# Kernel optimization log

Hardware: AMD Instinct MI355X
Metric: run time of the kernel (lower is better)

Reference implementation:

```python
import jax, jax.numpy as jnp
import numpy as np

K = 9  # kernel_size (knn neighbors, loop=True -> self included)

def setup_inputs() -> dict:
    key = jax.random.key(0)
    k1, k2, k3 = jax.random.split(key, 3)
    B, C, H, W = 8, 64, 32, 32
    OUT = 64
    x = jax.random.normal(k1, (B, C, H, W), dtype=jnp.float32)
    # SAGEConv params: lin_l (neighbor aggregate, with bias), lin_r (root, no bias)
    s = 1.0 / np.sqrt(C)
    W_l = jax.random.uniform(k2, (OUT, C), minval=-s, maxval=s, dtype=jnp.float32)
    b_l = jnp.zeros((OUT,), dtype=jnp.float32)
    W_r = jax.random.uniform(k3, (OUT, C), minval=-s, maxval=s, dtype=jnp.float32)
    return {"x": x, "W_l": W_l, "b_l": b_l, "W_r": W_r}

def _knn_mean(x_f, batches):
    # squared-euclidean pairwise distances [N, N], masked across batches
    sq = jnp.sum(x_f * x_f, axis=-1)
    dist = sq[:, None] + sq[None, :] - 2.0 * (x_f @ x_f.T)
    cross = batches[:, None] != batches[None, :]
    dist = jnp.where(cross, jnp.inf, dist)
    neg, idx = jax.lax.top_k(-dist, K)          # k nearest (self included, dist 0)
    valid = (neg != -jnp.inf).astype(x_f.dtype)  # handle degenerate last-batch node
    nbr = x_f[idx] * valid[..., None]            # [N, K, C]
    return nbr.sum(axis=1) / valid.sum(axis=1, keepdims=True)

def reference(x, W_l, b_l, W_r):
    B, C, H, Wd = x.shape
    N = B * H * Wd
    x_f = x.transpose(0, 2, 3, 1).reshape(N, C)  # flat_nodes: [B*H*W, C]
    # torch.linspace(0, B, steps=N).to(int64): truncation of i*B/(N-1)
    batches = jnp.linspace(0.0, float(B), N).astype(jnp.int32)
    mean_nbr = _knn_mean(x_f, batches)
    # SAGEConv: lin_l(mean_j x_j) + lin_r(x_i)
    return mean_nbr @ W_l.T + b_l + x_f @ W_r.T
```

## Files before the change

kernel.cpp:

```cpp
#include <hip/hip_runtime.h>
#include <cstdint>
#include <cstddef>


#define CBUF_HW (64 * 1028)
#define CBUF_BYTES (CBUF_HW * 2)

__device__ __forceinline__ unsigned mono32(float d) {
  unsigned u = __float_as_uint(d);
  return (u & 0x80000000u) ? ~u : (u | 0x80000000u);
}

__device__ __forceinline__ unsigned bmin32(unsigned v) {
#pragma unroll
  for (int off = 32; off; off >>= 1) {
    unsigned o = (unsigned)__shfl_xor((int)v, off, 64);
    v = (o < v) ? o : v;
  }
  return v;
}

__device__ __forceinline__ float rdlane(float v, int src) {
  return __int_as_float(__builtin_amdgcn_readlane(__float_as_int(v), src));
}

__device__ __forceinline__ unsigned short bf16rn(float v) {
  unsigned bits = __float_as_uint(v);
  return (unsigned short)((bits + 0x7FFFu + ((bits >> 16) & 1u)) >> 16);
}

extern "C" __global__ __launch_bounds__(256, 1)
void k_fused(const float* __restrict__ x,
             const float* __restrict__ Wl,
             const float* __restrict__ bl,
             const float* __restrict__ Wr,
             float* __restrict__ out) {
  extern __shared__ unsigned short cbuf[];
  int t = threadIdx.x;
  int lane = t & 63;
  int w = t >> 6;
  int n0 = (int)blockIdx.x << 5;
  int s = (n0 >= 7168) ? 7168 : (n0 & ~1023);
  int b = s >> 10;
  const float* xb = x + ((size_t)b << 16);

  float rowf[8];
#pragma unroll
  for (int r = 0; r < 8; ++r) {
    int n = n0 + (w << 3) + r;
    rowf[r] = xb[(lane << 10) + (n & 1023)];
  }

  float acc[8][16];
#pragma unroll
  for (int r = 0; r < 8; ++r)
#pragma unroll
    for (int q = 0; q < 16; ++q) acc[r][q] = 0.f;
  float sqc[16];
#pragma unroll
  for (int q = 0; q < 16; ++q) sqc[q] = 0.f;

  float4 cnd[2][4];
#pragma unroll
  for (int e = 0; e < 4; ++e)
    cnd[0][e] = *(const float4*)&xb[(lane << 2) + (e << 8)];

#pragma unroll 1
  for (int ch2 = 0; ch2 < 32; ++ch2) {
#pragma unroll
    for (int h = 0; h < 2; ++h) {
      int ch = (ch2 << 1) + h;
      int cur = ch & 1;
      if ((ch & 7) == 0) __syncthreads();
      int chn = (ch < 63) ? ch + 1 : 63;
#pragma unroll
      for (int e = 0; e < 4; ++e)
        cnd[cur ^ 1][e] = *(const float4*)&xb[(chn << 10) + (lane << 2) + (e << 8)];
      if ((ch >> 4) == w) {
#pragma unroll
        for (int e = 0; e < 4; ++e) {
          ushort4 pk;
          pk.x = bf16rn(cnd[cur][e].x);
          pk.y = bf16rn(cnd[cur][e].y);
          pk.z = bf16rn(cnd[cur][e].z);
          pk.w = bf16rn(cnd[cur][e].w);
          *(ushort4*)&cbuf[ch * 1028 + (lane << 2) + (e << 8)] = pk;
        }
      }
      float rv[8];
#pragma unroll
      for (int r = 0; r < 8; ++r) rv[r] = rdlane(rowf[r], ch);
#pragma unroll
      for (int e = 0; e < 4; ++e) {
        float cv[4] = {cnd[cur][e].x, cnd[cur][e].y, cnd[cur][e].z, cnd[cur][e].w};
#pragma unroll
        for (int j = 0; j < 4; ++j) {
          int q = (e << 2) + j;
          sqc[q] = fmaf(cv[j], cv[j], sqc[q]);
#pragma unroll
          for (int r = 0; r < 8; ++r)
            acc[r][q] = fmaf(rv[r], cv[j], acc[r][q]);
        }
      }
    }
  }
  __syncthreads();

  float ms[8];
#pragma unroll
  for (int r = 0; r < 8; ++r) {
    int n = n0 + (w << 3) + r;
    if (n == 8191) { ms[r] = rowf[r]; continue; }
    int lr = n - s;
    int lslot = (((lr >> 8) << 2) | (lr & 3));
    int llane = (lr >> 2) & 63;
    float sel = sqc[0];
#pragma unroll
    for (int q = 1; q < 16; ++q) sel = (q == lslot) ? sqc[q] : sel;
    float sqr = __shfl(sel, llane, 64);

    bool mrow = (s == 7168);
    unsigned d[16];
#pragma unroll
    for (int q = 0; q < 16; ++q)
      d[q] = mono32((sqr + sqc[q]) - 2.f * acc[r][q]);
    if (mrow && lane == 63) d[15] = 0xFFFFFFFFu;

    unsigned m1d = d[0], m2d = d[1];
    int m1s = 0, m2s = 1;
    if (m2d < m1d) { unsigned td = m1d; m1d = m2d; m2d = td; m1s = 1; m2s = 0; }
#pragma unroll
    for (int q = 2; q < 16; ++q) {
      unsigned dq = d[q];
      bool lt1 = dq < m1d, lt2 = dq < m2d;
      m2d = lt1 ? m1d : (lt2 ? dq : m2d);
      m2s = lt1 ? m1s : (lt2 ? q : m2s);
      m1d = lt1 ? dq : m1d;
      m1s = lt1 ? q : m1s;
    }
    unsigned lmd = m1d;
    int lms = m1s;
    unsigned rmask = 0;
    bool stale = false;
    float msum = 0.f;
#pragma unroll 1
    for (int kk = 0; kk < 9; ++kk) {
      unsigned g = bmin32(lmd);
      bool eq = (lmd == g);
      unsigned long long mask = __ballot(eq);
      unsigned cc = ((unsigned)lane << 2) | ((unsigned)(lms >> 2) << 8) | (unsigned)(lms & 3);
      unsigned wc;
      if (__popcll(mask) == 1) {
        wc = (unsigned)__shfl((int)cc, (int)(__ffsll((long long)mask) - 1), 64);
      } else {
        unsigned tc = eq ? cc : 0xFFFFFFFFu;
        wc = bmin32(tc);
      }
      msum += __uint_as_float((unsigned)cbuf[lane * 1028 + (int)wc] << 16);
      if (eq && cc == wc) {
        rmask |= 1u << lms;
        if (!stale) { lmd = m2d; lms = m2s; stale = true; }
        else {
          unsigned bd = 0xFFFFFFFFu; int bs = 0;
#pragma unroll
          for (int q = 0; q < 16; ++q) {
            bool alive = ((rmask >> q) & 1u) == 0u;
            bool take = alive && (d[q] < bd);
            bd = take ? d[q] : bd;
            bs = take ? q : bs;
          }
          lmd = bd; lms = bs;
        }
      }
    }
    ms[r] = msum / 9.0f;
  }

  float4 wl4[16], wr4[16];
#pragma unroll
  for (int k = 0; k < 16; ++k) {
    wl4[k] = *(const float4*)&Wl[(lane << 6) + (k << 2)];
    wr4[k] = *(const float4*)&Wr[(lane << 6) + (k << 2)];
  }
  float bias = bl[lane];
#pragma unroll 1
  for (int r = 0; r < 8; ++r) {
    int n = n0 + (w << 3) + r;
    float accL = 0.f, accR = 0.f;
#pragma unroll
    for (int c = 0; c < 64; ++c) {
      float mc = rdlane(ms[r], c);
      float xc = rdlane(rowf[r], c);
      const float* wlp = (const float*)&wl4[c >> 2];
      const float* wrp = (const float*)&wr4[c >> 2];
      accL = fmaf(mc, wlp[c & 3], accL);
      accR = fmaf(xc, wrp[c & 3], accR);
    }
    out[((size_t)n << 6) + lane] = accL + accR + bias;
  }
}

extern "C" void kernel_launch(void* const* d_in, const int* in_sizes, int n_in,
                              void* d_out, int out_size, void* d_ws, size_t ws_size,
                              hipStream_t stream) {
  const float* x  = (const float*)d_in[0];
  const float* Wl = (const float*)d_in[1];
  const float* bl = (const float*)d_in[2];
  const float* Wr = (const float*)d_in[3];
  float* out = (float*)d_out;

  hipFuncSetAttribute((const void*)k_fused,
                      hipFuncAttributeMaxDynamicSharedMemorySize, CBUF_BYTES);
  k_fused<<<256, 256, CBUF_BYTES, stream>>>(x, Wl, bl, Wr, out);
}
```

Baseline: 118.6 us.

## Interleave top-k selection across eight rows and prefetch two channels per step

The top-9 selection loop now processes all eight rows of a warp together, interleaving their butterfly shuffle reductions so the independent shuffle chains can overlap instead of running serially per row. The tie-break path always uses a second min-reduction rather than branching on ballot popcount. The candidate prefetch is restructured to load two channels per outer iteration, and the periodic __syncthreads inside the distance loop is removed. This raises register pressure (8x16 distance array kept live), and dropping the barriers relies on only the final sync before the LDS reads.

```diff
diff --git a/kernel.cpp b/kernel.cpp
--- a/kernel.cpp
+++ b/kernel.cpp
@@ -3,21 +3,12 @@
 #include <cstddef>
 
 
-#define CBUF_HW (64 * 1028)
-#define CBUF_BYTES (CBUF_HW * 2)
+#define CBUF_STRIDE 1028
+#define CBUF_BYTES (64 * CBUF_STRIDE * 2)
 
 __device__ __forceinline__ unsigned mono32(float d) {
   unsigned u = __float_as_uint(d);
   return (u & 0x80000000u) ? ~u : (u | 0x80000000u);
-}
-
-__device__ __forceinline__ unsigned bmin32(unsigned v) {
-#pragma unroll
-  for (int off = 32; off; off >>= 1) {
-    unsigned o = (unsigned)__shfl_xor((int)v, off, 64);
-    v = (o < v) ? o : v;
-  }
-  return v;
 }
 
 __device__ __forceinline__ float rdlane(float v, int src) {
@@ -41,8 +32,7 @@
   int w = t >> 6;
   int n0 = (int)blockIdx.x << 5;
   int s = (n0 >= 7168) ? 7168 : (n0 & ~1023);
-  int b = s >> 10;
-  const float* xb = x + ((size_t)b << 16);
+  const float* xb = x + ((size_t)(s >> 10) << 16);
 
   float rowf[8];
 #pragma unroll
@@ -60,31 +50,37 @@
 #pragma unroll
   for (int q = 0; q < 16; ++q) sqc[q] = 0.f;
 
-  float4 cnd[2][4];
-#pragma unroll
-  for (int e = 0; e < 4; ++e)
-    cnd[0][e] = *(const float4*)&xb[(lane << 2) + (e << 8)];
+  float4 pb[2][2][4];
+#pragma unroll
+  for (int h = 0; h < 2; ++h)
+#pragma unroll
+    for (int e = 0; e < 4; ++e)
+      pb[0][h][e] = *(const float4*)&xb[(h << 10) + (lane << 2) + (e << 8)];
 
 #pragma unroll 1
   for (int ch2 = 0; ch2 < 32; ++ch2) {
+    int cur = ch2 & 1;
+    if (ch2 < 31) {
+      int chn = (ch2 << 1) + 2;
+#pragma unroll
+      for (int h = 0; h < 2; ++h)
+#pragma unroll
+        for (int e = 0; e < 4; ++e)
+          pb[cur ^ 1][h][e] =
+              *(const float4*)&xb[((chn + h) << 10) + (lane << 2) + (e << 8)];
+    }
 #pragma unroll
     for (int h = 0; h < 2; ++h) {
       int ch = (ch2 << 1) + h;
-      int cur = ch & 1;
-      if ((ch & 7) == 0) __syncthreads();
-      int chn = (ch < 63) ? ch + 1 : 63;
-#pragma unroll
-      for (int e = 0; e < 4; ++e)
-        cnd[cur ^ 1][e] = *(const float4*)&xb[(chn << 10) + (lane << 2) + (e << 8)];
       if ((ch >> 4) == w) {
 #pragma unroll
         for (int e = 0; e < 4; ++e) {
           ushort4 pk;
-          pk.x = bf16rn(cnd[cur][e].x);
-          pk.y = bf16rn(cnd[cur][e].y);
-          pk.z = bf16rn(cnd[cur][e].z);
-          pk.w = bf16rn(cnd[cur][e].w);
-          *(ushort4*)&cbuf[ch * 1028 + (lane << 2) + (e << 8)] = pk;
+          pk.x = bf16rn(pb[cur][h][e].x);
+          pk.y = bf16rn(pb[cur][h][e].y);
+          pk.z = bf16rn(pb[cur][h][e].z);
+          pk.w = bf16rn(pb[cur][h][e].w);
+          *(ushort4*)&cbuf[ch * CBUF_STRIDE + (lane << 2) + (e << 8)] = pk;
         }
       }
       float rv[8];
@@ -92,7 +88,7 @@
       for (int r = 0; r < 8; ++r) rv[r] = rdlane(rowf[r], ch);
 #pragma unroll
       for (int e = 0; e < 4; ++e) {
-        float cv[4] = {cnd[cur][e].x, cnd[cur][e].y, cnd[cur][e].z, cnd[cur][e].w};
+        float cv[4] = {pb[cur][h][e].x, pb[cur][h][e].y, pb[cur][h][e].z, pb[cur][h][e].w};
 #pragma unroll
         for (int j = 0; j < 4; ++j) {
           int q = (e << 2) + j;
@@ -106,74 +102,116 @@
   }
   __syncthreads();
 
-  float ms[8];
-#pragma unroll
-  for (int r = 0; r < 8; ++r) {
-    int n = n0 + (w << 3) + r;
-    if (n == 8191) { ms[r] = rowf[r]; continue; }
-    int lr = n - s;
-    int lslot = (((lr >> 8) << 2) | (lr & 3));
+  float sqr[8];
+#pragma unroll
+  for (int r = 0; r < 8; ++r) {
+    int lr = (n0 + (w << 3) + r) - s;
+    int lslot = ((lr >> 8) << 2) | (lr & 3);
     int llane = (lr >> 2) & 63;
     float sel = sqc[0];
 #pragma unroll
     for (int q = 1; q < 16; ++q) sel = (q == lslot) ? sqc[q] : sel;
-    float sqr = __shfl(sel, llane, 64);
-
-    bool mrow = (s == 7168);
-    unsigned d[16];
+    sqr[r] = __shfl(sel, llane, 64);
+  }
+
+  bool mrow = (s == 7168);
+  unsigned du[8][16];
+#pragma unroll
+  for (int r = 0; r < 8; ++r)
 #pragma unroll
     for (int q = 0; q < 16; ++q)
-      d[q] = mono32((sqr + sqc[q]) - 2.f * acc[r][q]);
-    if (mrow && lane == 63) d[15] = 0xFFFFFFFFu;
-
-    unsigned m1d = d[0], m2d = d[1];
-    int m1s = 0, m2s = 1;
-    if (m2d < m1d) { unsigned td = m1d; m1d = m2d; m2d = td; m1s = 1; m2s = 0; }
+      du[r][q] = mono32((sqr[r] + sqc[q]) - 2.f * acc[r][q]);
+  if (mrow && lane == 63)
+#pragma unroll
+    for (int r = 0; r < 8; ++r) du[r][15] = 0xFFFFFFFFu;
+
+  unsigned m1d[8], m2d[8];
+  int m1s[8], m2s[8];
+#pragma unroll
+  for (int r = 0; r < 8; ++r) {
+    unsigned a = du[r][0], b = du[r][1];
+    if (b < a) { m1d[r] = b; m2d[r] = a; m1s[r] = 1; m2s[r] = 0; }
+    else       { m1d[r] = a; m2d[r] = b; m1s[r] = 0; m2s[r] = 1; }
 #pragma unroll
     for (int q = 2; q < 16; ++q) {
-      unsigned dq = d[q];
-      bool lt1 = dq < m1d, lt2 = dq < m2d;
-      m2d = lt1 ? m1d : (lt2 ? dq : m2d);
-      m2s = lt1 ? m1s : (lt2 ? q : m2s);
-      m1d = lt1 ? dq : m1d;
-      m1s = lt1 ? q : m1s;
-    }
-    unsigned lmd = m1d;
-    int lms = m1s;
-    unsigned rmask = 0;
-    bool stale = false;
-    float msum = 0.f;
+      unsigned dq = du[r][q];
+      bool lt1 = dq < m1d[r], lt2 = dq < m2d[r];
+      m2d[r] = lt1 ? m1d[r] : (lt2 ? dq : m2d[r]);
+      m2s[r] = lt1 ? m1s[r] : (lt2 ? q : m2s[r]);
+      m1d[r] = lt1 ? dq : m1d[r];
+      m1s[r] = lt1 ? q : m1s[r];
+    }
+  }
+
+  unsigned lmd[8], rmask[8];
+  int lms[8];
+  unsigned staleM = 0;
+  float msum[8];
+#pragma unroll
+  for (int r = 0; r < 8; ++r) {
+    lmd[r] = m1d[r]; lms[r] = m1s[r]; rmask[r] = 0u; msum[r] = 0.f;
+  }
+
 #pragma unroll 1
-    for (int kk = 0; kk < 9; ++kk) {
-      unsigned g = bmin32(lmd);
-      bool eq = (lmd == g);
-      unsigned long long mask = __ballot(eq);
-      unsigned cc = ((unsigned)lane << 2) | ((unsigned)(lms >> 2) << 8) | (unsigned)(lms & 3);
-      unsigned wc;
-      if (__popcll(mask) == 1) {
-        wc = (unsigned)__shfl((int)cc, (int)(__ffsll((long long)mask) - 1), 64);
-      } else {
-        unsigned tc = eq ? cc : 0xFFFFFFFFu;
-        wc = bmin32(tc);
-      }
-      msum += __uint_as_float((unsigned)cbuf[lane * 1028 + (int)wc] << 16);
-      if (eq && cc == wc) {
-        rmask |= 1u << lms;
-        if (!stale) { lmd = m2d; lms = m2s; stale = true; }
-        else {
+  for (int kk = 0; kk < 9; ++kk) {
+    unsigned g[8];
+#pragma unroll
+    for (int r = 0; r < 8; ++r) g[r] = lmd[r];
+#pragma unroll
+    for (int off = 32; off; off >>= 1) {
+#pragma unroll
+      for (int r = 0; r < 8; ++r) {
+        unsigned o = (unsigned)__shfl_xor((int)g[r], off, 64);
+        g[r] = (o < g[r]) ? o : g[r];
+      }
+    }
+    unsigned wc[8];
+#pragma unroll
+    for (int r = 0; r < 8; ++r) {
+      unsigned cc = ((unsigned)lane << 2) | ((unsigned)(lms[r] >> 2) << 8) |
+                    (unsigned)(lms[r] & 3);
+      wc[r] = (lmd[r] == g[r]) ? cc : 0xFFFFFFFFu;
+    }
+#pragma unroll
+    for (int off = 32; off; off >>= 1) {
+#pragma unroll
+      for (int r = 0; r < 8; ++r) {
+        unsigned o = (unsigned)__shfl_xor((int)wc[r], off, 64);
+        wc[r] = (o < wc[r]) ? o : wc[r];
+      }
+    }
+#pragma unroll
+    for (int r = 0; r < 8; ++r)
+      msum[r] += __uint_as_float(
+          (unsigned)cbuf[lane * CBUF_STRIDE + (int)(wc[r] & 1023u)] << 16);
+#pragma unroll
+    for (int r = 0; r < 8; ++r) {
+      unsigned cc = ((unsigned)lane << 2) | ((unsigned)(lms[r] >> 2) << 8) |
+                    (unsigned)(lms[r] & 3);
+      if (lmd[r] == g[r] && cc == wc[r]) {
+        rmask[r] |= 1u << lms[r];
+        if (!((staleM >> r) & 1u)) {
+          lmd[r] = m2d[r]; lms[r] = m2s[r]; staleM |= 1u << r;
+        } else {
           unsigned bd = 0xFFFFFFFFu; int bs = 0;
 #pragma unroll
           for (int q = 0; q < 16; ++q) {
-            bool alive = ((rmask >> q) & 1u) == 0u;
-            bool take = alive && (d[q] < bd);
-            bd = take ? d[q] : bd;
+            bool alive = ((rmask[r] >> q) & 1u) == 0u;
+            bool take = alive && (du[r][q] < bd);
+            bd = take ? du[r][q] : bd;
             bs = take ? q : bs;
           }
-          lmd = bd; lms = bs;
+          lmd[r] = bd; lms[r] = bs;
         }
       }
     }
-    ms[r] = msum / 9.0f;
+  }
+
+  float ms[8];
+#pragma unroll
+  for (int r = 0; r < 8; ++r) {
+    int n = n0 + (w << 3) + r;
+    ms[r] = (n == 8191) ? rowf[r] : msum[r] / 9.0f;
   }
 
   float4 wl4[16], wr4[16];
```

After: 155.9 us. +31.5%, slower.

## Split each block's rows across 16 waves instead of 4

Applied to the files above, without the earlier changes.

The block grows from 256 to 1024 threads, so each wave handles 2 query rows instead of 8 while the block still covers 32 rows. The distance accumulators, top-9 selection loop and output projection are rewritten for 2 rows per wave, which cuts per-wave register use and the serial per-row selection work. The aim is to hide latency with 16 resident waves per CU. The cost is that every wave now streams the full candidate tile from global memory, so redundant loads quadruple, and barriers now span 16 waves.

```diff
diff --git a/kernel.cpp b/kernel.cpp
--- a/kernel.cpp
+++ b/kernel.cpp
@@ -3,8 +3,8 @@
 #include <cstddef>
 
 
-#define CBUF_HW (64 * 1028)
-#define CBUF_BYTES (CBUF_HW * 2)
+#define CBUF_STRIDE 1028
+#define CBUF_BYTES (64 * CBUF_STRIDE * 2)
 
 __device__ __forceinline__ unsigned mono32(float d) {
   unsigned u = __float_as_uint(d);
@@ -29,7 +29,7 @@
   return (unsigned short)((bits + 0x7FFFu + ((bits >> 16) & 1u)) >> 16);
 }
 
-extern "C" __global__ __launch_bounds__(256, 1)
+extern "C" __global__ __launch_bounds__(1024, 4)
 void k_fused(const float* __restrict__ x,
              const float* __restrict__ Wl,
              const float* __restrict__ bl,
@@ -40,90 +40,88 @@
   int lane = t & 63;
   int w = t >> 6;
   int n0 = (int)blockIdx.x << 5;
-  int s = (n0 >= 7168) ? 7168 : (n0 & ~1023);
-  int b = s >> 10;
-  const float* xb = x + ((size_t)b << 16);
-
-  float rowf[8];
-#pragma unroll
-  for (int r = 0; r < 8; ++r) {
-    int n = n0 + (w << 3) + r;
+  int s = n0 & ~1023;
+  const float* xb = x + ((size_t)(s >> 10) << 16);
+
+  float rowf[2];
+#pragma unroll
+  for (int r = 0; r < 2; ++r) {
+    int n = n0 + (w << 1) + r;
     rowf[r] = xb[(lane << 10) + (n & 1023)];
   }
 
-  float acc[8][16];
-#pragma unroll
-  for (int r = 0; r < 8; ++r)
+  float acc[2][16];
+#pragma unroll
+  for (int r = 0; r < 2; ++r)
 #pragma unroll
     for (int q = 0; q < 16; ++q) acc[r][q] = 0.f;
   float sqc[16];
 #pragma unroll
   for (int q = 0; q < 16; ++q) sqc[q] = 0.f;
 
-  float4 cnd[2][4];
+  float4 cur[4], nxt[4];
 #pragma unroll
   for (int e = 0; e < 4; ++e)
-    cnd[0][e] = *(const float4*)&xb[(lane << 2) + (e << 8)];
+    cur[e] = *(const float4*)&xb[(lane << 2) + (e << 8)];
 
 #pragma unroll 1
-  for (int ch2 = 0; ch2 < 32; ++ch2) {
-#pragma unroll
-    for (int h = 0; h < 2; ++h) {
-      int ch = (ch2 << 1) + h;
-      int cur = ch & 1;
-      if ((ch & 7) == 0) __syncthreads();
-      int chn = (ch < 63) ? ch + 1 : 63;
+  for (int ch = 0; ch < 64; ++ch) {
+    if (ch < 63) {
 #pragma unroll
       for (int e = 0; e < 4; ++e)
-        cnd[cur ^ 1][e] = *(const float4*)&xb[(chn << 10) + (lane << 2) + (e << 8)];
-      if ((ch >> 4) == w) {
-#pragma unroll
-        for (int e = 0; e < 4; ++e) {
-          ushort4 pk;
-          pk.x = bf16rn(cnd[cur][e].x);
-          pk.y = bf16rn(cnd[cur][e].y);
-          pk.z = bf16rn(cnd[cur][e].z);
-          pk.w = bf16rn(cnd[cur][e].w);
-          *(ushort4*)&cbuf[ch * 1028 + (lane << 2) + (e << 8)] = pk;
-        }
-      }
-      float rv[8];
-#pragma unroll
-      for (int r = 0; r < 8; ++r) rv[r] = rdlane(rowf[r], ch);
+        nxt[e] = *(const float4*)&xb[((ch + 1) << 10) + (lane << 2) + (e << 8)];
+    }
+    if ((ch >> 2) == w) {
 #pragma unroll
       for (int e = 0; e < 4; ++e) {
-        float cv[4] = {cnd[cur][e].x, cnd[cur][e].y, cnd[cur][e].z, cnd[cur][e].w};
-#pragma unroll
-        for (int j = 0; j < 4; ++j) {
-          int q = (e << 2) + j;
-          sqc[q] = fmaf(cv[j], cv[j], sqc[q]);
-#pragma unroll
-          for (int r = 0; r < 8; ++r)
-            acc[r][q] = fmaf(rv[r], cv[j], acc[r][q]);
-        }
-      }
-    }
+        ushort4 pk;
+        pk.x = bf16rn(cur[e].x);
+        pk.y = bf16rn(cur[e].y);
+        pk.z = bf16rn(cur[e].z);
+        pk.w = bf16rn(cur[e].w);
+        *(ushort4*)&cbuf[ch * CBUF_STRIDE + (lane << 2) + (e << 8)] = pk;
+      }
+    }
+    float rv0 = rdlane(rowf[0], ch);
+    float rv1 = rdlane(rowf[1], ch);
+#pragma unroll
+    for (int e = 0; e < 4; ++e) {
+      float cv[4] = {cur[e].x, cur[e].y, cur[e].z, cur[e].w};
+#pragma unroll
+      for (int j = 0; j < 4; ++j) {
+        int q = (e << 2) + j;
+        sqc[q] = fmaf(cv[j], cv[j], sqc[q]);
+        acc[0][q] = fmaf(rv0, cv[j], acc[0][q]);
+        acc[1][q] = fmaf(rv1, cv[j], acc[1][q]);
+      }
+    }
+#pragma unroll
+    for (int e = 0; e < 4; ++e) cur[e] = nxt[e];
+    if ((ch & 7) == 7) __syncthreads();
   }
   __syncthreads();
 
-  float ms[8];
-#pragma unroll
-  for (int r = 0; r < 8; ++r) {
-    int n = n0 + (w << 3) + r;
-    if (n == 8191) { ms[r] = rowf[r]; continue; }
+  bool mrow = (s == 7168);
+  float ms[2];
+#pragma unroll 1
+  for (int r = 0; r < 2; ++r) {
+    int n = n0 + (w << 1) + r;
+    float rf = (r == 0) ? rowf[0] : rowf[1];
+    if (n == 8191) { ms[r] = rf; continue; }
     int lr = n - s;
-    int lslot = (((lr >> 8) << 2) | (lr & 3));
+    int lslot = ((lr >> 8) << 2) | (lr & 3);
     int llane = (lr >> 2) & 63;
     float sel = sqc[0];
 #pragma unroll
     for (int q = 1; q < 16; ++q) sel = (q == lslot) ? sqc[q] : sel;
     float sqr = __shfl(sel, llane, 64);
 
-    bool mrow = (s == 7168);
     unsigned d[16];
 #pragma unroll
-    for (int q = 0; q < 16; ++q)
-      d[q] = mono32((sqr + sqc[q]) - 2.f * acc[r][q]);
+    for (int q = 0; q < 16; ++q) {
+      float a = (r == 0) ? acc[0][q] : acc[1][q];
+      d[q] = mono32((sqr + sqc[q]) - 2.f * a);
+    }
     if (mrow && lane == 63) d[15] = 0xFFFFFFFFu;
 
     unsigned m1d = d[0], m2d = d[1];
@@ -148,7 +146,8 @@
       unsigned g = bmin32(lmd);
       bool eq = (lmd == g);
       unsigned long long mask = __ballot(eq);
-      unsigned cc = ((unsigned)lane << 2) | ((unsigned)(lms >> 2) << 8) | (unsigned)(lms & 3);
+      unsigned cc = ((unsigned)lane << 2) | ((unsigned)(lms >> 2) << 8) |
+                    (unsigned)(lms & 3);
       unsigned wc;
       if (__popcll(mask) == 1) {
         wc = (unsigned)__shfl((int)cc, (int)(__ffsll((long long)mask) - 1), 64);
@@ -156,7 +155,8 @@
         unsigned tc = eq ? cc : 0xFFFFFFFFu;
         wc = bmin32(tc);
       }
-      msum += __uint_as_float((unsigned)cbuf[lane * 1028 + (int)wc] << 16);
+      msum += __uint_as_float(
+          (unsigned)cbuf[lane * CBUF_STRIDE + (int)wc] << 16);
       if (eq && cc == wc) {
         rmask |= 1u << lms;
         if (!stale) { lmd = m2d; lms = m2s; stale = true; }
@@ -176,27 +176,39 @@
     ms[r] = msum / 9.0f;
   }
 
-  float4 wl4[16], wr4[16];
-#pragma unroll
-  for (int k = 0; k < 16; ++k) {
-    wl4[k] = *(const float4*)&Wl[(lane << 6) + (k << 2)];
-    wr4[k] = *(const float4*)&Wr[(lane << 6) + (k << 2)];
+  float accL[2] = {0.f, 0.f};
+  {
+    float4 wq[16];
+#pragma unroll
+    for (int k = 0; k < 16; ++k)
+      wq[k] = *(const float4*)&Wl[(lane << 6) + (k << 2)];
+#pragma unroll
+    for (int c = 0; c < 64; ++c) {
+      const float* wp = (const float*)&wq[c >> 2];
+      float wv = wp[c & 3];
+      accL[0] = fmaf(rdlane(ms[0], c), wv, accL[0]);
+      accL[1] = fmaf(rdlane(ms[1], c), wv, accL[1]);
+    }
+  }
+  float accR[2] = {0.f, 0.f};
+  {
+    float4 wq[16];
+#pragma unroll
+    for (int k = 0; k < 16; ++k)
+      wq[k] = *(const float4*)&Wr[(lane << 6) + (k << 2)];
+#pragma unroll
+    for (int c = 0; c < 64; ++c) {
+      const float* wp = (const float*)&wq[c >> 2];
+      float wv = wp[c & 3];
+      accR[0] = fmaf(rdlane(rowf[0], c), wv, accR[0]);
+      accR[1] = fmaf(rdlane(rowf[1], c), wv, accR[1]);
+    }
   }
   float bias = bl[lane];
-#pragma unroll 1
-  for (int r = 0; r < 8; ++r) {
-    int n = n0 + (w << 3) + r;
-    float accL = 0.f, accR = 0.f;
-#pragma unroll
-    for (int c = 0; c < 64; ++c) {
-      float mc = rdlane(ms[r], c);
-      float xc = rdlane(rowf[r], c);
-      const float* wlp = (const float*)&wl4[c >> 2];
-      const float* wrp = (const float*)&wr4[c >> 2];
-      accL = fmaf(mc, wlp[c & 3], accL);
-      accR = fmaf(xc, wrp[c & 3], accR);
-    }
-    out[((size_t)n << 6) + lane] = accL + accR + bias;
+#pragma unroll
+  for (int r = 0; r < 2; ++r) {
+    int n = n0 + (w << 1) + r;
+    out[((size_t)n << 6) + lane] = accL[r] + accR[r] + bias;
   }
 }
 
@@ -211,5 +223,5 @@
 
   hipFuncSetAttribute((const void*)k_fused,
                       hipFuncAttributeMaxDynamicSharedMemorySize, CBUF_BYTES);
-  k_fused<<<256, 256, CBUF_BYTES, stream>>>(x, Wl, bl, Wr, out);
-}
+  k_fused<<<256, 1024, CBUF_BYTES, stream>>>(x, Wl, bl, Wr, out);
+}
```

After: 115.9 us. 1.02x faster.
